# Performance work log

Measured on AMD Instinct MI355X. Metric: run time of the kernel, lower is better.

Reference implementation:

```python
import jax, jax.numpy as jnp
import numpy as np

RADIUS = 0.4
K = 32
EPS = 1e-5


def ball_query(xyz, new_xyz, radius, k):
    """xyz: (B,N,3), new_xyz: (B,M,3) -> idx (B,M,k) int32.
    Replicates CUDA ball_query: first k points within radius (in index order),
    padded with the first found index."""
    N = xyz.shape[1]
    # squared distances (B,M,N)
    d2 = jnp.sum((new_xyz[:, :, None, :] - xyz[:, None, :, :]) ** 2, axis=-1)
    within = d2 < radius * radius
    order = jnp.arange(N, dtype=jnp.int32)
    key = jnp.where(within, order[None, None, :], N)
    idx_sorted = jnp.argsort(key, axis=-1)[..., :k].astype(jnp.int32)  # (B,M,k)
    cnt = within.sum(axis=-1)  # (B,M)
    first = idx_sorted[..., :1]
    slot = jnp.arange(k)[None, None, :]
    return jnp.where(slot < cnt[..., None], idx_sorted, first)


def gather_bmk(x_bnc, idx):
    """x_bnc: (B,N,C), idx: (B,M,K) -> (B,M,K,C)"""
    return jnp.take_along_axis(x_bnc[:, None, :, :], idx[..., None], axis=2)


def conv_bn_relu(x, w, b, gamma, beta):
    """x: (B,Cin,M,K); w: (Cout,Cin). 1x1 Conv2d + BatchNorm2d (train stats) + ReLU."""
    x = jnp.einsum('bcmk,oc->bomk', x, w) + b[None, :, None, None]
    mu = x.mean(axis=(0, 2, 3), keepdims=True)
    var = x.var(axis=(0, 2, 3), keepdims=True)
    x = gamma[None, :, None, None] * (x - mu) * jax.lax.rsqrt(var + EPS) + beta[None, :, None, None]
    return jax.nn.relu(x)


def setup_inputs() -> dict:
    key = jax.random.key(0)
    ks = jax.random.split(key, 16)
    B, N, C, M = 4, 16384, 128, 1024
    mlp = [131, 128, 128, 256]
    inp = {
        'points_xyz': jax.random.normal(ks[0], (B, N, 3), dtype=jnp.float32),
        'features': jax.random.normal(ks[1], (B, C, N), dtype=jnp.float32),
        'indices': jax.random.randint(ks[2], (B, M), 0, N, dtype=jnp.int32),
    }
    for i in range(3):
        cin, cout = mlp[i], mlp[i + 1]
        inp[f'w{i+1}'] = jax.random.normal(ks[3 + 4 * i], (cout, cin), dtype=jnp.float32) / np.sqrt(cin)
        inp[f'b{i+1}'] = jnp.zeros((cout,), dtype=jnp.float32)
        inp[f'g{i+1}'] = jnp.ones((cout,), dtype=jnp.float32)
        inp[f'beta{i+1}'] = jnp.zeros((cout,), dtype=jnp.float32)
    return inp


def reference(points_xyz, features, indices,
              w1, b1, g1, beta1, w2, b2, g2, beta2, w3, b3, g3, beta3):
    # sample centers: new_xyz (B,M,3)
    new_xyz = jnp.take_along_axis(points_xyz, indices[..., None], axis=1)
    # ball query + group
    idx = ball_query(points_xyz, new_xyz, RADIUS, K)            # (B,M,K)
    grouped_xyz = gather_bmk(points_xyz, idx) - new_xyz[:, :, None, :]  # (B,M,K,3)
    grouped_feat = gather_bmk(features.transpose(0, 2, 1), idx)         # (B,M,K,C)
    x = jnp.concatenate([grouped_xyz, grouped_feat], axis=-1)           # (B,M,K,3+C)
    x = x.transpose(0, 3, 1, 2)                                         # (B,3+C,M,K)
    # shared MLP (1x1 Conv2d + BN + ReLU)
    x = conv_bn_relu(x, w1, b1, g1, beta1)
    x = conv_bn_relu(x, w2, b2, g2, beta2)
    x = conv_bn_relu(x, w3, b3, g3, beta3)
    # max pool over K -> (B, Cout, M)
    new_features = x.max(axis=-1)
    return new_xyz, new_features
```

## Files before the change

kernel.cpp:

```cpp
#include <hip/hip_runtime.h>

#define B_ 4
#define N_ 16384
#define C_ 128
#define M_ 1024
#define K_ 32
#define NTOT (B_*M_*K_)
#define RAD2 0.16f
#define EPS_ 1e-5f

typedef unsigned short ushort_t;
typedef __bf16 bf16x8 __attribute__((ext_vector_type(8)));
typedef float f32x4 __attribute__((ext_vector_type(4)));

__device__ __forceinline__ float b2f(ushort_t u){
  unsigned int x = ((unsigned int)u) << 16;
  return __builtin_bit_cast(float, x);
}
__device__ __forceinline__ ushort_t f2b(float f){
  return __builtin_bit_cast(ushort_t, (__bf16)f);
}

__global__ __launch_bounds__(256) void prep_all_k(
    const float* __restrict__ feat, ushort_t* __restrict__ ftr_t,
    const float* __restrict__ xyz, const int* __restrict__ indices,
    float* __restrict__ new_xyz, int* __restrict__ idx,
    const float* __restrict__ w1, const float* __restrict__ w2, const float* __restrict__ w3,
    ushort_t* __restrict__ W1b, ushort_t* __restrict__ W2b, ushort_t* __restrict__ W3b,
    float* __restrict__ stats)
{
  __shared__ float T[32][133];
  int bid = blockIdx.x;
  int t = threadIdx.x;

  if (bid < 2048){
    int b = bid >> 9, ntile = bid & 511;
    int n0 = ntile * 32;
    int nl = t & 31;
    #pragma unroll
    for (int ci = 0; ci < 16; ci++){
      int c = ci*8 + (t >> 5);
      T[nl][c] = feat[((size_t)b*C_ + c)*N_ + n0 + nl];
    }
    __syncthreads();
    #pragma unroll
    for (int ii = 0; ii < 2; ii++){
      int v = ii*256 + t;
      int n2 = v >> 4, seg = v & 15;
      union { ushort_t u[8]; uint4 q; } pk;
      #pragma unroll
      for (int j = 0; j < 8; j++) pk.u[j] = f2b(T[n2][seg*8 + j]);
      *(uint4*)(ftr_t + ((size_t)b*N_ + n0 + n2)*C_ + seg*8) = pk.q;
    }
  } else if (bid < 3072){
    int wv = t >> 6, lane = t & 63;
    int g = (bid - 2048)*4 + wv;
    int b = g >> 10;
    const float* pb = xyz + (size_t)b*N_*3;
    const float4* pb4 = (const float4*)pb;
    int qi = indices[g];
    float qx = pb[qi*3+0], qy = pb[qi*3+1], qz = pb[qi*3+2];
    if (lane < 3) new_xyz[g*3 + lane] = pb[qi*3 + lane];

    int cnt = 0, firstIdx = 0;
    int* op = idx + g*K_;

    float4 buf0[6], buf1[6];
    #pragma unroll
    for (int i = 0; i < 6; i++) buf0[i] = pb4[lane*6 + i];

    auto process = [&](const float4* buf, int chunk){
      const float* f = (const float*)buf;
      unsigned int local_mask = 0;
      #pragma unroll
      for (int j = 0; j < 8; j++){
        float dx = f[j*3+0]-qx, dy = f[j*3+1]-qy, dz = f[j*3+2]-qz;
        if (dx*dx + dy*dy + dz*dz < RAD2) local_mask |= (1u << j);
      }
      if (__ballot(local_mask != 0) == 0ull) return;
      int base = chunk*512;
      int lcnt = __popc(local_mask);
      int incl = lcnt;
      #pragma unroll
      for (int d = 1; d < 64; d <<= 1){
        int tt = __shfl_up(incl, d);
        if (lane >= d) incl += tt;
      }
      int excl = incl - lcnt;
      int total = __shfl(incl, 63);
      if (cnt == 0){
        int lf = local_mask ? (lane*8 + __builtin_ctz(local_mask)) : 0x7fffffff;
        #pragma unroll
        for (int d = 1; d < 64; d <<= 1) lf = min(lf, __shfl_xor(lf, d));
        firstIdx = base + lf;
      }
      int sl = cnt + excl;
      unsigned int m = local_mask;
      while (m && sl < K_){
        int j = __builtin_ctz(m); m &= m - 1u;
        op[sl++] = base + lane*8 + j;
      }
      cnt += total;
    };

    for (int chunk = 0; chunk < 32; chunk += 2){
      if (chunk + 1 < 32){
        #pragma unroll
        for (int i = 0; i < 6; i++) buf1[i] = pb4[(chunk+1)*384 + lane*6 + i];
      }
      process(buf0, chunk);
      if (cnt >= K_) break;
      if (chunk + 2 < 32){
        #pragma unroll
        for (int i = 0; i < 6; i++) buf0[i] = pb4[(chunk+2)*384 + lane*6 + i];
      }
      process(buf1, chunk + 1);
      if (cnt >= K_) break;
    }
    if (cnt < K_){
      for (int s = cnt + lane; s < K_; s += 64) op[s] = firstIdx;
    }
  } else {
    const int T1 = 128*160, T2 = 128*128;
    int e = (bid - 3072)*256 + t;
    if (e < T1){
      int o = e / 160, c = e % 160;
      float v = 0.f;
      if (c < 128) v = w1[o*131 + 3 + c];
      else if (c < 131) v = w1[o*131 + (c - 128)];
      W1b[e] = f2b(v);
    } else if (e < T1+T2){
      int e2 = e - T1;
      W2b[e2] = f2b(w2[e2]);
    } else {
      int e3 = e - T1 - T2;
      W3b[e3] = f2b(w3[e3]);
    }
    if (bid == 3072){
      #pragma unroll
      for (int j = 0; j < 6; j++) stats[j*256 + t] = 0.f;
    }
  }
}

__global__ __launch_bounds__(256, 2) void conv1_k(
    const float* __restrict__ xyz, const ushort_t* __restrict__ ftr_t,
    const int* __restrict__ idx, const float* __restrict__ new_xyz,
    const ushort_t* __restrict__ W1b, const float* __restrict__ b1,
    ushort_t* __restrict__ Y1, float* __restrict__ sumO, float* __restrict__ sqO)
{
  __shared__ alignas(16) ushort_t Xs[2][32*168];
  __shared__ alignas(16) float Ys[2][32*68];
  int t = threadIdx.x;
  int wv = t >> 6, lane = t & 63, quad = lane >> 4, l15 = lane & 15;
  int row = t >> 3, chunk = t & 7;
  int col0 = (blockIdx.x & 1) * 64;
  int blk = blockIdx.x >> 1;

  if (t < 128){
    int rr = t >> 2, cc = t & 3;
    *(uint4*)(Xs[0] + rr*168 + 128 + cc*8) = make_uint4(0,0,0,0);
    *(uint4*)(Xs[1] + rr*168 + 128 + cc*8) = make_uint4(0,0,0,0);
  }
  bf16x8 wf[5];
  #pragma unroll
  for (int kt = 0; kt < 5; kt++)
    wf[kt] = *(const bf16x8*)(W1b + (col0 + wv*16 + l15)*160 + kt*32 + quad*8);
  float bs_r = b1[col0 + wv*16 + l15];
  float s = 0.f, s2 = 0.f;

  const int GPB = 8;
  int g0 = blk * GPB;
  int b = g0 >> 10;
  int ia[GPB], ibv[GPB];
  #pragma unroll
  for (int i = 0; i < GPB; i++){
    ia[i]  = idx[(g0+i)*K_ + row];
    ibv[i] = idx[(g0+i)*K_ + (t & 31)];
  }
  uint4 r0, r1;
  float p3x, p3y, p3z, q3x, q3y, q3z;
  {
    const ushort_t* src = ftr_t + ((size_t)b*N_ + ia[0])*C_ + chunk*16;
    r0 = *(const uint4*)src; r1 = *(const uint4*)(src + 8);
    if (t < 32){
      const float* pp = xyz + ((size_t)b*N_ + ibv[0])*3;
      const float* qq = new_xyz + (size_t)g0*3;
      p3x = pp[0]; p3y = pp[1]; p3z = pp[2];
      q3x = qq[0]; q3y = qq[1]; q3z = qq[2];
    }
  }
  for (int i = 0; i < GPB; i++){
    int p = i & 1;
    ushort_t* X = Xs[p];
    *(uint4*)(X + row*168 + chunk*16) = r0;
    *(uint4*)(X + row*168 + chunk*16 + 8) = r1;
    if (t < 32){
      unsigned int u0 = (unsigned int)f2b(p3x-q3x) | ((unsigned int)f2b(p3y-q3y) << 16);
      unsigned int u1 = (unsigned int)f2b(p3z-q3z);
      *(uint2*)(X + t*168 + 128) = make_uint2(u0, u1);
    }
    if (i + 1 < GPB){
      const ushort_t* src = ftr_t + ((size_t)b*N_ + ia[i+1])*C_ + chunk*16;
      r0 = *(const uint4*)src; r1 = *(const uint4*)(src + 8);
      if (t < 32){
        const float* pp = xyz + ((size_t)b*N_ + ibv[i+1])*3;
        const float* qq = new_xyz + (size_t)(g0+i+1)*3;
        p3x = pp[0]; p3y = pp[1]; p3z = pp[2];
        q3x = qq[0]; q3y = qq[1]; q3z = qq[2];
      }
    }
    __syncthreads();
    bf16x8 af[2][5];
    #pragma unroll
    for (int mt = 0; mt < 2; mt++)
      #pragma unroll
      for (int kt = 0; kt < 5; kt++)
        af[mt][kt] = *(const bf16x8*)(X + (mt*16 + l15)*168 + kt*32 + quad*8);
    f32x4 acc[2] = {(f32x4){0,0,0,0}, (f32x4){0,0,0,0}};
    #pragma unroll
    for (int kt = 0; kt < 5; kt++){
      acc[0] = __builtin_amdgcn_mfma_f32_16x16x32_bf16(af[0][kt], wf[kt], acc[0], 0,0,0);
      acc[1] = __builtin_amdgcn_mfma_f32_16x16x32_bf16(af[1][kt], wf[kt], acc[1], 0,0,0);
    }
    {
      int o = wv*16 + l15;
      float* Yw = Ys[p];
      #pragma unroll
      for (int mt = 0; mt < 2; mt++)
        #pragma unroll
        for (int r = 0; r < 4; r++){
          float v = acc[mt][r] + bs_r;
          s += v; s2 += v*v;
          Yw[(mt*16 + quad*4 + r)*68 + o] = v;
        }
    }
    if (i > 0){
      const float* yp = &Ys[p^1][row*68 + chunk*8];
      f32x4 y0 = *(const f32x4*)(yp);
      f32x4 y1 = *(const f32x4*)(yp + 4);
      union { ushort_t u[8]; uint4 q; } p0;
      #pragma unroll
      for (int j = 0; j < 4; j++){
        p0.u[j] = f2b(y0[j]); p0.u[4+j] = f2b(y1[j]);
      }
      *(uint4*)(Y1 + ((size_t)(g0+i-1)*K_ + row)*128 + col0 + chunk*8) = p0.q;
    }
  }
  __syncthreads();
  {
    const float* yp = &Ys[(GPB-1)&1][row*68 + chunk*8];
    f32x4 y0 = *(const f32x4*)(yp);
    f32x4 y1 = *(const f32x4*)(yp + 4);
    union { ushort_t u[8]; uint4 q; } p0;
    #pragma unroll
    for (int j = 0; j < 4; j++){
      p0.u[j] = f2b(y0[j]); p0.u[4+j] = f2b(y1[j]);
    }
    *(uint4*)(Y1 + ((size_t)(g0+GPB-1)*K_ + row)*128 + col0 + chunk*8) = p0.q;
  }
  s  += __shfl_xor(s, 16);  s  += __shfl_xor(s, 32);
  s2 += __shfl_xor(s2, 16); s2 += __shfl_xor(s2, 32);
  if (quad == 0){
    int o = col0 + wv*16 + l15;
    atomicAdd(&sumO[o], s);
    atomicAdd(&sqO[o], s2);
  }
}

template<int COUT, bool MAXMIN>
__global__ __launch_bounds__(256, 2) void convB_k(
    const ushort_t* __restrict__ Yin, const ushort_t* __restrict__ Wb,
    const float* __restrict__ bias, const float* __restrict__ g_bn,
    const float* __restrict__ beta_bn, const float* __restrict__ sumI,
    const float* __restrict__ sqI, ushort_t* __restrict__ Yout,
    unsigned int* __restrict__ Ymm, float* __restrict__ sumO, float* __restrict__ sqO)
{
  constexpr int HALF = COUT/2;
  constexpr int NT = HALF/64;
  __shared__ alignas(16) ushort_t Xs[2][32*136];
  __shared__ alignas(16) float Ys[MAXMIN ? 1 : 2][MAXMIN ? 4 : 32*68];
  int t = threadIdx.x;
  int wv = t >> 6, lane = t & 63, quad = lane >> 4, l15 = lane & 15;
  int row = t >> 3, chunk = t & 7;
  int col0 = (blockIdx.x & 1) * HALF;
  int blk = blockIdx.x >> 1;

  float a_r[16], d_r[16];
  #pragma unroll
  for (int j = 0; j < 16; j++){
    int c = chunk*16 + j;
    float mu  = sumI[c] * (1.f/NTOT);
    float var = sqI[c]  * (1.f/NTOT) - mu*mu;
    float a = g_bn[c] * rsqrtf(var + EPS_);
    a_r[j] = a; d_r[j] = beta_bn[c] - a*mu;
  }
  bf16x8 wf[NT][4];
  #pragma unroll
  for (int nt = 0; nt < NT; nt++)
    #pragma unroll
    for (int kt = 0; kt < 4; kt++)
      wf[nt][kt] = *(const bf16x8*)(Wb + (col0 + wv*(NT*16) + nt*16 + l15)*128 + kt*32 + quad*8);
  float bs_r[NT];
  #pragma unroll
  for (int nt = 0; nt < NT; nt++) bs_r[nt] = bias[col0 + wv*(NT*16) + nt*16 + l15];
  float s[NT], s2[NT];
  #pragma unroll
  for (int nt = 0; nt < NT; nt++){ s[nt] = 0.f; s2[nt] = 0.f; }

  const int GPB = 8;
  int g0 = blk * GPB;
  uint4 r0, r1;
  {
    const ushort_t* src = Yin + ((size_t)g0*K_ + row)*128 + chunk*16;
    r0 = *(const uint4*)src; r1 = *(const uint4*)(src + 8);
  }
  for (int i = 0; i < GPB; i++){
    int p = i & 1;
    int g = g0 + i;
    ushort_t* X = Xs[p];
    union { ushort_t u[8]; uint4 q; } i0, i1, o0, o1;
    i0.q = r0; i1.q = r1;
    #pragma unroll
    for (int j = 0; j < 8; j++){
      o0.u[j] = f2b(fmaxf(a_r[j]  *b2f(i0.u[j]) + d_r[j],   0.f));
      o1.u[j] = f2b(fmaxf(a_r[8+j]*b2f(i1.u[j]) + d_r[8+j], 0.f));
    }
    *(uint4*)(X + row*136 + chunk*16) = o0.q;
    *(uint4*)(X + row*136 + chunk*16 + 8) = o1.q;
    if (i + 1 < GPB){
      const ushort_t* src = Yin + ((size_t)(g+1)*K_ + row)*128 + chunk*16;
      r0 = *(const uint4*)src; r1 = *(const uint4*)(src + 8);
    }
    __syncthreads();
    bf16x8 af[2][4];
    #pragma unroll
    for (int mt = 0; mt < 2; mt++)
      #pragma unroll
      for (int kt = 0; kt < 4; kt++)
        af[mt][kt] = *(const bf16x8*)(X + (mt*16 + l15)*136 + kt*32 + quad*8);
    f32x4 acc[NT][2];
    #pragma unroll
    for (int nt = 0; nt < NT; nt++){ acc[nt][0] = (f32x4){0,0,0,0}; acc[nt][1] = (f32x4){0,0,0,0}; }
    #pragma unroll
    for (int nt = 0; nt < NT; nt++)
      #pragma unroll
      for (int kt = 0; kt < 4; kt++){
        acc[nt][0] = __builtin_amdgcn_mfma_f32_16x16x32_bf16(af[0][kt], wf[nt][kt], acc[nt][0], 0,0,0);
        acc[nt][1] = __builtin_amdgcn_mfma_f32_16x16x32_bf16(af[1][kt], wf[nt][kt], acc[nt][1], 0,0,0);
      }
    if constexpr (!MAXMIN){
      {
        int o = wv*16 + l15;
        float* Yw = Ys[p];
        #pragma unroll
        for (int mt = 0; mt < 2; mt++)
          #pragma unroll
          for (int r = 0; r < 4; r++){
            float v = acc[0][mt][r] + bs_r[0];
            s[0] += v; s2[0] += v*v;
            Yw[(mt*16 + quad*4 + r)*68 + o] = v;
          }
      }
      if (i > 0){
        const float* yp = &Ys[p^1][row*68 + chunk*8];
        f32x4 y0 = *(const f32x4*)(yp);
        f32x4 y1 = *(const f32x4*)(yp + 4);
        union { ushort_t u[8]; uint4 q; } p0;
        #pragma unroll
        for (int j = 0; j < 4; j++){
          p0.u[j] = f2b(y0[j]); p0.u[4+j] = f2b(y1[j]);
        }
        *(uint4*)(Yout + ((size_t)(g-1)*K_ + row)*128 + col0 + chunk*8) = p0.q;
      }
    } else {
      #pragma unroll
      for (int nt = 0; nt < NT; nt++){
        float v0 = acc[nt][0][0] + bs_r[nt];
        float mx = v0, mn = v0;
        s[nt] += v0; s2[nt] += v0*v0;
        #pragma unroll
        for (int mt = 0; mt < 2; mt++)
          #pragma unroll
          for (int r = 0; r < 4; r++){
            if (mt == 0 && r == 0) continue;
            float v = acc[nt][mt][r] + bs_r[nt];
            s[nt] += v; s2[nt] += v*v;
            mx = fmaxf(mx, v); mn = fminf(mn, v);
          }
        mx = fmaxf(mx, __shfl_xor(mx, 16)); mx = fmaxf(mx, __shfl_xor(mx, 32));
        mn = fminf(mn, __shfl_xor(mn, 16)); mn = fminf(mn, __shfl_xor(mn, 32));
        if (quad == 0){
          int o = col0 + wv*(NT*16) + nt*16 + l15;
          Ymm[(size_t)g*256 + o] = (unsigned int)f2b(mx) | ((unsigned int)f2b(mn) << 16);
        }
      }
    }
  }
  if constexpr (!MAXMIN){
    __syncthreads();
    const float* yp = &Ys[(GPB-1)&1][row*68 + chunk*8];
    f32x4 y0 = *(const f32x4*)(yp);
    f32x4 y1 = *(const f32x4*)(yp + 4);
    union { ushort_t u[8]; uint4 q; } p0;
    #pragma unroll
    for (int j = 0; j < 4; j++){
      p0.u[j] = f2b(y0[j]); p0.u[4+j] = f2b(y1[j]);
    }
    *(uint4*)(Yout + ((size_t)(g0+GPB-1)*K_ + row)*128 + col0 + chunk*8) = p0.q;
  }
  #pragma unroll
  for (int nt = 0; nt < NT; nt++){
    s[nt]  += __shfl_xor(s[nt], 16);  s[nt]  += __shfl_xor(s[nt], 32);
    s2[nt] += __shfl_xor(s2[nt], 16); s2[nt] += __shfl_xor(s2[nt], 32);
    if (quad == 0){
      int o = col0 + wv*(NT*16) + nt*16 + l15;
      atomicAdd(&sumO[o], s[nt]);
      atomicAdd(&sqO[o], s2[nt]);
    }
  }
}

__global__ __launch_bounds__(256) void finalize_k(
    const unsigned int* __restrict__ Ymm, const float* __restrict__ g3,
    const float* __restrict__ beta3, const float* __restrict__ sum3,
    const float* __restrict__ sq3, float* __restrict__ out)
{
  __shared__ float T[16][264];
  __shared__ float abn[256], dbn[256];
  int t = threadIdx.x;
  int b = blockIdx.x >> 6;
  int m0 = (blockIdx.x & 63) * 16;
  {
    float mu  = sum3[t] * (1.f/NTOT);
    float var = sq3[t]  * (1.f/NTOT) - mu*mu;
    float a = g3[t] * rsqrtf(var + EPS_);
    abn[t] = a; dbn[t] = beta3[t] - a*mu;
  }
  __syncthreads();
  #pragma unroll
  for (int i = 0; i < 4; i++){
    int v4 = i*256 + t;
    int m = v4 >> 6, oq = (v4 & 63) * 4;
    uint4 w = *(const uint4*)(Ymm + ((size_t)(b*M_ + m0 + m))*256 + oq);
    unsigned int wsv[4] = {w.x, w.y, w.z, w.w};
    float r[4];
    #pragma unroll
    for (int j = 0; j < 4; j++){
      int o = oq + j;
      float mx = b2f((ushort_t)(wsv[j] & 0xffffu));
      float mn = b2f((ushort_t)(wsv[j] >> 16));
      float a = abn[o];
      float val = (a >= 0.f) ? (a*mx + dbn[o]) : (a*mn + dbn[o]);
      r[j] = fmaxf(val, 0.f);
    }
    *(f32x4*)(&T[m][oq]) = *(f32x4*)r;
  }
  __syncthreads();
  #pragma unroll
  for (int p = 0; p < 4; p++){
    int o = p*64 + (t >> 2), c = t & 3;
    float4 v = make_float4(T[c*4+0][o], T[c*4+1][o], T[c*4+2][o], T[c*4+3][o]);
    *(float4*)(out + ((size_t)(b*256 + o))*M_ + m0 + c*4) = v;
  }
}

extern "C" void kernel_launch(void* const* d_in, const int* in_sizes, int n_in,
                              void* d_out, int out_size, void* d_ws, size_t ws_size,
                              hipStream_t stream)
{
  (void)in_sizes; (void)n_in; (void)out_size; (void)ws_size;
  const float* xyz  = (const float*)d_in[0];
  const float* feat = (const float*)d_in[1];
  const int*   inds = (const int*)d_in[2];
  const float* w1 = (const float*)d_in[3];
  const float* b1 = (const float*)d_in[4];
  const float* g1 = (const float*)d_in[5];
  const float* be1= (const float*)d_in[6];
  const float* w2 = (const float*)d_in[7];
  const float* b2 = (const float*)d_in[8];
  const float* g2 = (const float*)d_in[9];
  const float* be2= (const float*)d_in[10];
  const float* w3 = (const float*)d_in[11];
  const float* b3 = (const float*)d_in[12];
  const float* g3 = (const float*)d_in[13];
  const float* be3= (const float*)d_in[14];

  char* ws = (char*)d_ws;
  float* stats = (float*)ws;
  float* s1sum = stats + 0*256;  float* s1sq = stats + 1*256;
  float* s2sum = stats + 2*256;  float* s2sq = stats + 3*256;
  float* s3sum = stats + 4*256;  float* s3sq = stats + 5*256;
  size_t off = 6*256*sizeof(float);
  int* idx = (int*)(ws + off);                off += (size_t)B_*M_*K_*4;
  ushort_t* ftr_t = (ushort_t*)(ws + off);    off += (size_t)B_*N_*C_*2;
  ushort_t* W1b = (ushort_t*)(ws + off);      off += 128*160*2;
  ushort_t* W2b = (ushort_t*)(ws + off);      off += 128*128*2;
  ushort_t* W3b = (ushort_t*)(ws + off);      off += 256*128*2;
  ushort_t* Y1 = (ushort_t*)(ws + off);       off += (size_t)NTOT*128*2;
  ushort_t* Y2 = (ushort_t*)(ws + off);       off += (size_t)NTOT*128*2;
  unsigned int* Ymm = (unsigned int*)(ws + off); off += (size_t)B_*M_*256*4;

  float* new_xyz  = (float*)d_out;
  float* out_feat = (float*)d_out + (size_t)B_*M_*3;

  prep_all_k<<<3344, 256, 0, stream>>>(feat, ftr_t, xyz, inds, new_xyz, idx,
                                       w1, w2, w3, W1b, W2b, W3b, stats);
  conv1_k<<<1024, 256, 0, stream>>>(xyz, ftr_t, idx, new_xyz, W1b, b1, Y1, s1sum, s1sq);
  convB_k<128,false><<<1024, 256, 0, stream>>>(Y1, W2b, b2, g1, be1, s1sum, s1sq, Y2, nullptr, s2sum, s2sq);
  convB_k<256,true ><<<1024, 256, 0, stream>>>(Y2, W3b, b3, g2, be2, s2sum, s2sq, nullptr, Ymm, s3sum, s3sq);
  finalize_k<<<256, 256, 0, stream>>>(Ymm, g3, be3, s3sum, s3sq, out_feat);
}
```

Baseline: 217.6 us.

## Split ball query across four waves per query with shared-memory merge

Each ball query now gets a full 256-thread block instead of one wave. The four waves scan disjoint quarters of the point cloud in parallel, write their hits into shared memory, and stop early once the earlier segments already hold K hits. A final merge writes the indices in order and pads the rest with the first hit. Ball-query blocks are also placed ahead of the feature-transpose blocks so the long-latency scans start first. The cost is more blocks, extra shared-memory traffic, block-wide syncs, and wasted scanning in later segments when earlier ones fill quickly.

```diff
diff --git a/kernel.cpp b/kernel.cpp
--- a/kernel.cpp
+++ b/kernel.cpp
@@ -30,44 +30,31 @@
     float* __restrict__ stats)
 {
   __shared__ float T[32][133];
+  __shared__ int seg_idx[4][32];
+  __shared__ int seg_cnt[4];
   int bid = blockIdx.x;
   int t = threadIdx.x;
 
-  if (bid < 2048){
-    int b = bid >> 9, ntile = bid & 511;
-    int n0 = ntile * 32;
-    int nl = t & 31;
-    #pragma unroll
-    for (int ci = 0; ci < 16; ci++){
-      int c = ci*8 + (t >> 5);
-      T[nl][c] = feat[((size_t)b*C_ + c)*N_ + n0 + nl];
-    }
-    __syncthreads();
-    #pragma unroll
-    for (int ii = 0; ii < 2; ii++){
-      int v = ii*256 + t;
-      int n2 = v >> 4, seg = v & 15;
-      union { ushort_t u[8]; uint4 q; } pk;
-      #pragma unroll
-      for (int j = 0; j < 8; j++) pk.u[j] = f2b(T[n2][seg*8 + j]);
-      *(uint4*)(ftr_t + ((size_t)b*N_ + n0 + n2)*C_ + seg*8) = pk.q;
-    }
-  } else if (bid < 3072){
-    int wv = t >> 6, lane = t & 63;
-    int g = (bid - 2048)*4 + wv;
+  if (bid < 4096){
+    int g = bid;
     int b = g >> 10;
     const float* pb = xyz + (size_t)b*N_*3;
     const float4* pb4 = (const float4*)pb;
     int qi = indices[g];
     float qx = pb[qi*3+0], qy = pb[qi*3+1], qz = pb[qi*3+2];
-    if (lane < 3) new_xyz[g*3 + lane] = pb[qi*3 + lane];
-
-    int cnt = 0, firstIdx = 0;
+    if (t < 3) new_xyz[g*3 + t] = pb[qi*3 + t];
+    int wv = t >> 6, lane = t & 63;
     int* op = idx + g*K_;
 
+    volatile int* scnt = seg_cnt;
+    if (lane == 0) scnt[wv] = 0;
+    __syncthreads();
+
+    int cnt = 0;
+    int base4 = wv*3072;
     float4 buf0[6], buf1[6];
     #pragma unroll
-    for (int i = 0; i < 6; i++) buf0[i] = pb4[lane*6 + i];
+    for (int i = 0; i < 6; i++) buf0[i] = pb4[base4 + lane*6 + i];
 
     auto process = [&](const float4* buf, int chunk){
       const float* f = (const float*)buf;
@@ -78,7 +65,7 @@
         if (dx*dx + dy*dy + dz*dz < RAD2) local_mask |= (1u << j);
       }
       if (__ballot(local_mask != 0) == 0ull) return;
-      int base = chunk*512;
+      int base = wv*4096 + chunk*512;
       int lcnt = __popc(local_mask);
       int incl = lcnt;
       #pragma unroll
@@ -88,41 +75,79 @@
       }
       int excl = incl - lcnt;
       int total = __shfl(incl, 63);
-      if (cnt == 0){
-        int lf = local_mask ? (lane*8 + __builtin_ctz(local_mask)) : 0x7fffffff;
-        #pragma unroll
-        for (int d = 1; d < 64; d <<= 1) lf = min(lf, __shfl_xor(lf, d));
-        firstIdx = base + lf;
-      }
       int sl = cnt + excl;
       unsigned int m = local_mask;
       while (m && sl < K_){
         int j = __builtin_ctz(m); m &= m - 1u;
-        op[sl++] = base + lane*8 + j;
+        seg_idx[wv][sl++] = base + lane*8 + j;
       }
       cnt += total;
+      if (lane == 0) scnt[wv] = (cnt < K_) ? cnt : K_;
     };
 
-    for (int chunk = 0; chunk < 32; chunk += 2){
-      if (chunk + 1 < 32){
+    for (int chunk = 0; chunk < 8; chunk += 2){
+      if (wv > 0){
+        int cum = 0;
+        for (int j = 0; j < wv; j++) cum += scnt[j];
+        if (cum >= K_) break;
+      }
+      if (chunk + 1 < 8){
         #pragma unroll
-        for (int i = 0; i < 6; i++) buf1[i] = pb4[(chunk+1)*384 + lane*6 + i];
+        for (int i = 0; i < 6; i++) buf1[i] = pb4[base4 + (chunk+1)*384 + lane*6 + i];
       }
       process(buf0, chunk);
       if (cnt >= K_) break;
-      if (chunk + 2 < 32){
+      if (chunk + 2 < 8){
         #pragma unroll
-        for (int i = 0; i < 6; i++) buf0[i] = pb4[(chunk+2)*384 + lane*6 + i];
+        for (int i = 0; i < 6; i++) buf0[i] = pb4[base4 + (chunk+2)*384 + lane*6 + i];
       }
       process(buf1, chunk + 1);
       if (cnt >= K_) break;
     }
-    if (cnt < K_){
-      for (int s = cnt + lane; s < K_; s += 64) op[s] = firstIdx;
+    __syncthreads();
+
+    int c0 = seg_cnt[0], c1 = seg_cnt[1], c2 = seg_cnt[2], c3 = seg_cnt[3];
+    if (t < 128){
+      int s = t >> 5, k2 = t & 31;
+      int off = (s == 0) ? 0 : (s == 1) ? c0 : (s == 2) ? c0+c1 : c0+c1+c2;
+      int cs  = (s == 0) ? c0 : (s == 1) ? c1 : (s == 2) ? c2 : c3;
+      if (k2 < cs){
+        int gs = off + k2;
+        if (gs < K_) op[gs] = seg_idx[s][k2];
+      }
+    }
+    int total = c0 + c1 + c2 + c3;
+    if (t < K_ && t >= total){
+      int firstIdx = 0;
+      if (c0) firstIdx = seg_idx[0][0];
+      else if (c1) firstIdx = seg_idx[1][0];
+      else if (c2) firstIdx = seg_idx[2][0];
+      else if (c3) firstIdx = seg_idx[3][0];
+      op[t] = firstIdx;
+    }
+  } else if (bid < 6144){
+    int bb = bid - 4096;
+    int b = bb >> 9, ntile = bb & 511;
+    int n0 = ntile * 32;
+    int nl = t & 31;
+    #pragma unroll
+    for (int ci = 0; ci < 16; ci++){
+      int c = ci*8 + (t >> 5);
+      T[nl][c] = feat[((size_t)b*C_ + c)*N_ + n0 + nl];
+    }
+    __syncthreads();
+    #pragma unroll
+    for (int ii = 0; ii < 2; ii++){
+      int v = ii*256 + t;
+      int n2 = v >> 4, seg = v & 15;
+      union { ushort_t u[8]; uint4 q; } pk;
+      #pragma unroll
+      for (int j = 0; j < 8; j++) pk.u[j] = f2b(T[n2][seg*8 + j]);
+      *(uint4*)(ftr_t + ((size_t)b*N_ + n0 + n2)*C_ + seg*8) = pk.q;
     }
   } else {
     const int T1 = 128*160, T2 = 128*128;
-    int e = (bid - 3072)*256 + t;
+    int e = (bid - 6144)*256 + t;
     if (e < T1){
       int o = e / 160, c = e % 160;
       float v = 0.f;
@@ -136,7 +161,7 @@
       int e3 = e - T1 - T2;
       W3b[e3] = f2b(w3[e3]);
     }
-    if (bid == 3072){
+    if (bid == 6144){
       #pragma unroll
       for (int j = 0; j < 6; j++) stats[j*256 + t] = 0.f;
     }
@@ -504,7 +529,7 @@
   float* new_xyz  = (float*)d_out;
   float* out_feat = (float*)d_out + (size_t)B_*M_*3;
 
-  prep_all_k<<<3344, 256, 0, stream>>>(feat, ftr_t, xyz, inds, new_xyz, idx,
+  prep_all_k<<<6416, 256, 0, stream>>>(feat, ftr_t, xyz, inds, new_xyz, idx,
                                        w1, w2, w3, W1b, W2b, W3b, stats);
   conv1_k<<<1024, 256, 0, stream>>>(xyz, ftr_t, idx, new_xyz, W1b, b1, Y1, s1sum, s1sq);
   convB_k<128,false><<<1024, 256, 0, stream>>>(Y1, W2b, b2, g1, be1, s1sum, s1sq, Y2, nullptr, s2sum, s2sq);
```

Result: no change. 219.0 us (+0.6%).
